# Kernel tuning notes

Hardware: AMD Instinct MI355X
Metric: run time of the kernel (lower is better)

The kernel has to match this reference:

```python
import jax, jax.numpy as jnp
import numpy as np

B, N, NS, D = 32, 1024, 8, 768
HID = max(D, 128)  # hidden_dim = max(dim, hidden_dim)
ITERS = 3
EPS = 1e-8        # slot-attention renorm eps
LN_EPS = 1e-5     # torch LayerNorm default
SCALE = D ** -0.5


def _layernorm(x, g, b):
    m = jnp.mean(x, axis=-1, keepdims=True)
    v = jnp.mean((x - m) ** 2, axis=-1, keepdims=True)
    return (x - m) * jax.lax.rsqrt(v + LN_EPS) * g + b


def setup_inputs() -> dict:
    key = jax.random.key(0)
    ks = jax.random.split(key, 12)

    def lin_w(k, fan_in, fan_out):
        # xavier-uniform-like init; stored as [in, out] for x @ W
        lim = np.sqrt(6.0 / (fan_in + fan_out)).astype(np.float32)
        return jax.random.uniform(k, (fan_in, fan_out), jnp.float32, -lim, lim)

    return {
        "slots": jax.random.normal(ks[0], (1, NS, D), jnp.float32),
        "inputs": jax.random.normal(ks[1], (B, N, D), jnp.float32),
        "Wq": lin_w(ks[2], D, D), "bq": jnp.zeros((D,), jnp.float32),
        "Wk": lin_w(ks[3], D, D), "bk": jnp.zeros((D,), jnp.float32),
        "Wv": lin_w(ks[4], D, D), "bv": jnp.zeros((D,), jnp.float32),
        "g_in": jnp.ones((D,), jnp.float32), "b_in": jnp.zeros((D,), jnp.float32),
        "g_s": jnp.ones((D,), jnp.float32), "b_s": jnp.zeros((D,), jnp.float32),
        "g_ff": jnp.ones((D,), jnp.float32), "b_ff": jnp.zeros((D,), jnp.float32),
        "W1": lin_w(ks[5], D, HID), "b1": jnp.zeros((HID,), jnp.float32),
        "W2": lin_w(ks[6], HID, D), "b2": jnp.zeros((D,), jnp.float32),
    }


def reference(slots, inputs, Wq, bq, Wk, bk, Wv, bv,
              g_in, b_in, g_s, b_s, g_ff, b_ff, W1, b1, W2, b2):
    b = inputs.shape[0]
    slots = jnp.broadcast_to(slots, (b,) + slots.shape[1:])  # [b, ns, d]

    x = _layernorm(inputs, g_in, b_in)
    k = x @ Wk + bk  # [b, n, d]
    v = x @ Wv + bv  # [b, n, d]

    attn = None
    for _ in range(ITERS):
        slots_prev = slots
        sn = _layernorm(slots, g_s, b_s)
        q = sn @ Wq + bq                                  # [b, ns, d]
        dots = jnp.einsum('bid,bjd->bij', q, k) * SCALE   # [b, ns, n]
        attn = jax.nn.softmax(dots, axis=1)               # softmax over slots
        attn = attn / (jnp.sum(attn, axis=-1, keepdims=True) + EPS)
        updates = jnp.einsum('bjd,bij->bid', v, attn)     # [b, ns, d]
        h = _layernorm(updates, g_ff, b_ff)
        slots = slots_prev + jax.nn.relu(h @ W1 + b1) @ W2 + b2 * 0 + (jax.nn.relu(h @ W1 + b1) @ W2 + b2 - (jax.nn.relu(h @ W1 + b1) @ W2)) * 0
        slots = slots_prev + (jax.nn.relu(h @ W1 + b1) @ W2 + b2)

    return slots, jnp.transpose(attn, (0, 2, 1))  # ([b,ns,d], [b,n,ns])
```

## Files before the change

kernel.cpp:

```cpp
#include <hip/hip_runtime.h>

#define LNEPS 1e-5f
#define AEPS 1e-8f
#define SCALE_Q 0.036084391824351615f

typedef unsigned int uint32;
typedef float f32x2 __attribute__((ext_vector_type(2)));

__device__ inline uint32 bfb(float f) {
  __bf16 h = (__bf16)f;
  unsigned short u;
  __builtin_memcpy(&u, &h, 2);
  return (uint32)u;
}
__device__ inline f32x2 unpk(uint32 u) {
  f32x2 v;
  v.x = __uint_as_float(u << 16);
  v.y = __uint_as_float(u & 0xffff0000u);
  return v;
}

__global__ void setup_k(const float* __restrict__ Wk, float* __restrict__ WkT,
                        const float* __restrict__ s0, float* __restrict__ slots) {
  __shared__ float tile[32][33];
  int bb = blockIdx.x, t = threadIdx.x;
  if (bb < 576) {
    int c0 = (bb % 24) * 32, i0 = (bb / 24) * 32;
    int tx = t & 31, ty = t >> 5;
#pragma unroll
    for (int k = 0; k < 4; ++k)
      tile[ty + 8 * k][tx] = Wk[(size_t)(i0 + ty + 8 * k) * 768 + c0 + tx];
    __syncthreads();
#pragma unroll
    for (int k = 0; k < 4; ++k)
      WkT[(size_t)(c0 + ty + 8 * k) * 768 + i0 + tx] = tile[tx][ty + 8 * k];
  } else {
    int idx = (bb - 576) * 256 + t;
    slots[idx] = s0[idx % 6144];
  }
}

template <bool LN, int MODE>
__global__ void gemv_k(const float* __restrict__ X, const float* __restrict__ W,
                       const float* __restrict__ bias, const float* __restrict__ gamma,
                       const float* __restrict__ beta_ln, const float* __restrict__ alpha,
                       const float* __restrict__ beta, float* __restrict__ out) {
  __shared__ float XsT[768 * 12];
  int t = threadIdx.x;
  int c0 = blockIdx.x * 64, r0 = blockIdx.y * 8;
#pragma unroll
  for (int j = 0; j < 3; ++j) {
    int fidx = j * 512 + t;
    int r = fidx / 192, c4 = fidx % 192;
    float4 v = *(const float4*)(X + (size_t)(r0 + r) * 768 + c4 * 4);
    int kb = c4 * 4;
    XsT[(kb + 0) * 12 + r] = v.x;
    XsT[(kb + 1) * 12 + r] = v.y;
    XsT[(kb + 2) * 12 + r] = v.z;
    XsT[(kb + 3) * 12 + r] = v.w;
  }
  __syncthreads();
  if (LN) {
    int w = t >> 6, l = t & 63;
    float s = 0.f, ss = 0.f;
#pragma unroll
    for (int m = 0; m < 12; ++m) {
      float x = XsT[(l + 64 * m) * 12 + w];
      s += x; ss += x * x;
    }
#pragma unroll
    for (int o = 32; o; o >>= 1) { s += __shfl_xor(s, o); ss += __shfl_xor(ss, o); }
    float mu = s * (1.f / 768.f), rs = rsqrtf(ss * (1.f / 768.f) - mu * mu + LNEPS);
#pragma unroll
    for (int m = 0; m < 12; ++m) {
      int d = l + 64 * m;
      XsT[d * 12 + w] = (XsT[d * 12 + w] - mu) * rs * gamma[d] + beta_ln[d];
    }
    __syncthreads();
  }
  int cx = t & 63, kg = t >> 6;
  int c = c0 + cx;
  float acc[8] = {};
  const float* wp = W + c;
  int k0 = kg * 96;
#pragma unroll 8
  for (int k = k0; k < k0 + 96; ++k) {
    float wv = wp[(size_t)k * 768];
    float4 xa = *(const float4*)&XsT[k * 12];
    float4 xb = *(const float4*)&XsT[k * 12 + 4];
    acc[0] += xa.x * wv; acc[1] += xa.y * wv; acc[2] += xa.z * wv; acc[3] += xa.w * wv;
    acc[4] += xb.x * wv; acc[5] += xb.y * wv; acc[6] += xb.z * wv; acc[7] += xb.w * wv;
  }
  __syncthreads();
  float* red = XsT;
  if (kg > 0) {
#pragma unroll
    for (int r = 0; r < 8; ++r) red[((kg - 1) * 8 + r) * 64 + cx] = acc[r];
  }
  __syncthreads();
  if (kg == 0) {
#pragma unroll
    for (int g = 1; g < 8; ++g)
#pragma unroll
      for (int r = 0; r < 8; ++r) acc[r] += red[((g - 1) * 8 + r) * 64 + cx];
    float bsc = (MODE == 1) ? 0.f : bias[c];
#pragma unroll
    for (int r = 0; r < 8; ++r) {
      int rr = r0 + r;
      size_t oidx = (size_t)rr * 768 + c;
      float v;
      if (MODE == 0) v = acc[r] + bsc;
      else if (MODE == 1) v = acc[r];
      else if (MODE == 2) v = acc[r] * alpha[rr] + bsc * beta[rr];
      else if (MODE == 3) v = fmaxf(acc[r] + bsc, 0.f);
      else v = out[oidx] + acc[r] + bsc;
      out[oidx] = v;
    }
  }
}

__global__ void qprep_k(const float* __restrict__ q, const float* __restrict__ qk,
                        const float* __restrict__ g_in, const float* __restrict__ b_in,
                        const float* __restrict__ bk, float* __restrict__ Sqbuf,
                        float* __restrict__ c0buf) {
  int row = blockIdx.x * 4 + (threadIdx.x >> 6), l = threadIdx.x & 63;
  float aS = 0.f, aC = 0.f;
#pragma unroll
  for (int j = 0; j < 12; ++j) {
    int d = l + 64 * j;
    float qkv = qk[(size_t)row * 768 + d];
    aS += qkv * g_in[d];
    aC += qkv * b_in[d] + q[(size_t)row * 768 + d] * bk[d];
  }
#pragma unroll
  for (int o = 32; o; o >>= 1) { aS += __shfl_xor(aS, o); aC += __shfl_xor(aC, o); }
  if (l == 0) { Sqbuf[row] = aS; c0buf[row] = aC; }
}

template <bool FIRST>
__global__ void __launch_bounds__(512, 2)
dotspool_k(const float* __restrict__ inf, uint32* __restrict__ xh,
           const float* __restrict__ qk, const float* __restrict__ g_in,
           const float* __restrict__ Sqbuf, const float* __restrict__ c0buf,
           float* __restrict__ attnbuf, uint32* __restrict__ partials,
           float* __restrict__ A0p, float* __restrict__ A1p) {
  __shared__ float qkgs[8][768];
  __shared__ uint32 xt[32 * 392];
  __shared__ float oa[64][8], ow[64][8], orm[64];
  __shared__ float c0s[8], Sqs[8];
  int chunk = blockIdx.x, b = blockIdx.y, t = threadIdx.x, w = t >> 6, l = t & 63;
  for (int i = t; i < 6144; i += 512)
    ((float*)qkgs)[i] = qk[(size_t)b * 6144 + i] * g_in[i % 768];
  if (t < 8) { c0s[t] = c0buf[b * 8 + t]; Sqs[t] = Sqbuf[b * 8 + t]; }
  int g32 = l & 31, grp = l >> 5;
  f32x2 pacc[8] = {};
#pragma unroll
  for (int sub = 0; sub < 2; ++sub) {
    if (FIRST) {
      const float4* xpf =
          (const float4*)(inf + ((size_t)b * 1024 + chunk * 64 + sub * 32) * 768);
      uint2* xg = (uint2*)(xh + ((size_t)b * 1024 + chunk * 64 + sub * 32) * 384);
#pragma unroll
      for (int j = 0; j < 12; ++j) {
        int idx = j * 512 + t;
        int row = idx / 192, c4 = idx % 192;
        float4 v = xpf[(size_t)row * 192 + c4];
        uint2 o;
        o.x = bfb(v.x) | (bfb(v.y) << 16);
        o.y = bfb(v.z) | (bfb(v.w) << 16);
        *(uint2*)&xt[row * 392 + c4 * 2] = o;
        xg[(size_t)row * 192 + c4] = o;
      }
    } else {
      const uint4* xps4 = (const uint4*)(xh + ((size_t)b * 1024 + chunk * 64) * 384 +
                                         sub * 12288);
#pragma unroll
      for (int j = 0; j < 6; ++j) {
        int idx = j * 512 + t;
        int row = idx / 96, c4 = idx % 96;
        *(uint4*)&xt[row * 392 + c4 * 4] = xps4[idx];
      }
    }
    __syncthreads();
#pragma unroll
    for (int rr = 0; rr < 2; ++rr) {
      int lr32 = rr * 16 + w * 2 + grp;
      int lr = sub * 32 + lr32;
      const uint32* xr = &xt[lr32 * 392];
      f32x2 sv = {0.f, 0.f}, ssv = {0.f, 0.f};
      f32x2 ds2[8] = {};
#pragma unroll 4
      for (int j = 0; j < 12; ++j) {
        uint32 u = xr[j * 32 + g32];
        f32x2 ab = unpk(u);
        sv += ab;
        ssv += ab * ab;
        int d0 = 2 * (j * 32 + g32);
#pragma unroll
        for (int s2 = 0; s2 < 8; ++s2) {
          f32x2 qg = *(const f32x2*)&qkgs[s2][d0];
          ds2[s2] += qg * ab;
        }
      }
      float s = sv.x + sv.y, ss = ssv.x + ssv.y;
      float ds[8];
#pragma unroll
      for (int s2 = 0; s2 < 8; ++s2) ds[s2] = ds2[s2].x + ds2[s2].y;
#pragma unroll
      for (int o = 1; o < 32; o <<= 1) {
        s += __shfl_xor(s, o);
        ss += __shfl_xor(ss, o);
#pragma unroll
        for (int s2 = 0; s2 < 8; ++s2) ds[s2] += __shfl_xor(ds[s2], o);
      }
      float mu = s * (1.f / 768.f), r = rsqrtf(ss * (1.f / 768.f) - mu * mu + LNEPS);
      float rmu = r * mu;
      float sc[8];
#pragma unroll
      for (int s2 = 0; s2 < 8; ++s2)
        sc[s2] = (r * ds[s2] - rmu * Sqs[s2] + c0s[s2]) * SCALE_Q;
      float mx = sc[0];
#pragma unroll
      for (int s2 = 1; s2 < 8; ++s2) mx = fmaxf(mx, sc[s2]);
      float e[8], se = 0.f;
#pragma unroll
      for (int s2 = 0; s2 < 8; ++s2) { e[s2] = __expf(sc[s2] - mx); se += e[s2]; }
      float inv_se = 1.f / se;
      float av = e[0];
#pragma unroll
      for (int s2 = 1; s2 < 8; ++s2) av = (g32 == s2) ? e[s2] : av;
      av *= inv_se;
      if (g32 < 8) {
        oa[lr][g32] = av;
        ow[lr][g32] = av * r;
      }
      if (g32 == 8) orm[lr] = rmu;
    }
    __syncthreads();
    if (t < 384) {
#pragma unroll 2
      for (int nn = 0; nn < 32; ++nn) {
        f32x2 xv = unpk(xt[nn * 392 + t]);
        const float* owr = &ow[sub * 32 + nn][0];
#pragma unroll
        for (int k = 0; k < 4; ++k) {
          f32x2 owv = *(const f32x2*)&owr[2 * k];
          pacc[2 * k] += owv.x * xv;
          pacc[2 * k + 1] += owv.y * xv;
        }
      }
    } else if (sub == 1 && t < 392) {
      int sl = t - 384;
      float A0 = 0.f, A1 = 0.f;
      for (int rr2 = 0; rr2 < 64; ++rr2) {
        float a = oa[rr2][sl];
        A0 += a;
        A1 += a * orm[rr2];
      }
      A0p[chunk * 256 + b * 8 + sl] = A0;
      A1p[chunk * 256 + b * 8 + sl] = A1;
    }
    __syncthreads();
  }
  if (t < 384) {
#pragma unroll
    for (int s2 = 0; s2 < 8; ++s2) {
      size_t base = ((size_t)(chunk * 256 + b * 8 + s2)) * 384;
      partials[base + t] = bfb(pacc[s2].x) | (bfb(pacc[s2].y) << 16);
    }
  }
  size_t base8 = ((size_t)b * 1024 + chunk * 64) * 8;
  attnbuf[base8 + t] = oa[t >> 3][t & 7];
}

__global__ void reduce_fix_k(const uint32* __restrict__ partials, const float* __restrict__ A0p,
                             const float* __restrict__ A1p, const float* __restrict__ g_in,
                             const float* __restrict__ b_in, float* __restrict__ pooled,
                             float* __restrict__ invbuf, float* __restrict__ rhobuf) {
  int row = blockIdx.x, t = threadIdx.x;
  float A0 = 0.f, A1 = 0.f;
#pragma unroll
  for (int ch = 0; ch < 16; ++ch) {
    A0 += A0p[ch * 256 + row];
    A1 += A1p[ch * 256 + row];
  }
  f32x2 a = {0.f, 0.f};
#pragma unroll
  for (int ch = 0; ch < 16; ++ch)
    a += unpk(partials[((size_t)(ch * 256 + row)) * 384 + t]);
  int d = 2 * t;
  f32x2 g = *(const f32x2*)&g_in[d];
  f32x2 bi = *(const f32x2*)&b_in[d];
  f32x2 res;
  res.x = g.x * (a.x - A1) + bi.x * A0;
  res.y = g.y * (a.y - A1) + bi.y * A0;
  *(f32x2*)&pooled[(size_t)row * 768 + d] = res;
  if (t == 0) {
    float iv = 1.f / (A0 + AEPS);
    invbuf[row] = iv;
    rhobuf[row] = A0 * iv;
  }
}

__global__ void outs_k(const float* __restrict__ slots, const float* __restrict__ attnbuf,
                       const float* __restrict__ invbuf, float* __restrict__ out) {
  int i = blockIdx.x * 256 + threadIdx.x;
  if (i < 196608) {
    out[i] = slots[i];
  } else {
    int j = i - 196608;
    out[i] = attnbuf[j] * invbuf[((j >> 13) << 3) + (j & 7)];
  }
}

extern "C" void kernel_launch(void* const* d_in, const int* in_sizes, int n_in,
                              void* d_out, int out_size, void* d_ws, size_t ws_size,
                              hipStream_t stream) {
  (void)in_sizes; (void)n_in; (void)out_size; (void)ws_size;
  const float* slots0 = (const float*)d_in[0];
  const float* inputs = (const float*)d_in[1];
  const float* Wq = (const float*)d_in[2];
  const float* bq = (const float*)d_in[3];
  const float* Wk = (const float*)d_in[4];
  const float* bk = (const float*)d_in[5];
  const float* Wv = (const float*)d_in[6];
  const float* bv = (const float*)d_in[7];
  const float* g_in = (const float*)d_in[8];
  const float* b_in = (const float*)d_in[9];
  const float* g_s = (const float*)d_in[10];
  const float* b_s = (const float*)d_in[11];
  const float* g_ff = (const float*)d_in[12];
  const float* b_ff = (const float*)d_in[13];
  const float* W1 = (const float*)d_in[14];
  const float* b1 = (const float*)d_in[15];
  const float* W2 = (const float*)d_in[16];
  const float* b2 = (const float*)d_in[17];

  char* p = (char*)d_ws;
  uint32* xh = (uint32*)p;     p += (size_t)32768 * 384 * 4;
  float* WkT = (float*)p;      p += (size_t)768 * 768 * 4;
  float* slotsf = (float*)p;   p += 256 * 768 * 4;
  float* qbuf = (float*)p;     p += 256 * 768 * 4;
  float* qkbuf = (float*)p;    p += 256 * 768 * 4;
  float* Sqbuf = (float*)p;    p += 256 * 4;
  float* c0buf = (float*)p;    p += 256 * 4;
  float* attnbuf = (float*)p;  p += (size_t)32768 * 8 * 4;
  uint32* partials = (uint32*)p; p += (size_t)16 * 256 * 384 * 4;
  float* A0p = (float*)p;      p += 16 * 256 * 4;
  float* A1p = (float*)p;      p += 16 * 256 * 4;
  float* pooled = (float*)p;   p += 256 * 768 * 4;
  float* invbuf = (float*)p;   p += 256 * 4;
  float* rhobuf = (float*)p;   p += 256 * 4;
  float* updbuf = (float*)p;   p += 256 * 768 * 4;
  float* t1buf = (float*)p;    p += 256 * 768 * 4;

  dim3 ggrid(12, 32);
  setup_k<<<1344, 256, 0, stream>>>(Wk, WkT, slots0, slotsf);
  for (int it = 0; it < 3; ++it) {
    gemv_k<true, 0><<<ggrid, 512, 0, stream>>>(slotsf, Wq, bq, g_s, b_s, nullptr, nullptr,
                                               qbuf);
    gemv_k<false, 1><<<ggrid, 512, 0, stream>>>(qbuf, WkT, nullptr, nullptr, nullptr, nullptr,
                                                nullptr, qkbuf);
    qprep_k<<<64, 256, 0, stream>>>(qbuf, qkbuf, g_in, b_in, bk, Sqbuf, c0buf);
    if (it == 0)
      dotspool_k<true><<<dim3(16, 32), 512, 0, stream>>>(inputs, xh, qkbuf, g_in, Sqbuf,
                                                         c0buf, attnbuf, partials, A0p, A1p);
    else
      dotspool_k<false><<<dim3(16, 32), 512, 0, stream>>>(inputs, xh, qkbuf, g_in, Sqbuf,
                                                          c0buf, attnbuf, partials, A0p, A1p);
    reduce_fix_k<<<256, 384, 0, stream>>>(partials, A0p, A1p, g_in, b_in, pooled,
                                          invbuf, rhobuf);
    gemv_k<false, 2><<<ggrid, 512, 0, stream>>>(pooled, Wv, bv, nullptr, nullptr, invbuf,
                                                rhobuf, updbuf);
    gemv_k<true, 3><<<ggrid, 512, 0, stream>>>(updbuf, W1, b1, g_ff, b_ff, nullptr, nullptr,
                                               t1buf);
    gemv_k<false, 4><<<ggrid, 512, 0, stream>>>(t1buf, W2, b2, nullptr, nullptr, nullptr,
                                                nullptr, slotsf);
  }
  outs_k<<<1792, 256, 0, stream>>>(slotsf, attnbuf, invbuf, (float*)d_out);
}
```

Measured before the change: 338.9 us.

## Cache per-row LayerNorm stats across iterations and shrink staging tile to 16 rows

The first iteration now writes each input row's LayerNorm mean and rstd to a workspace buffer, and later iterations read them back instead of recomputing the sum and sum of squares and their shuffle reductions. The dotspool loop also processes four sub-tiles of 16 rows, one row per 32-lane half-wave, in place of two 32-row sub-tiles, which cuts shared memory for the x tile and drops the row padding. The aim is less ALU and shuffle work per iteration and possibly better occupancy, at the cost of more barriers per block and a small extra global read. Removing the 392-word padding may add LDS bank conflicts in the pooling loop.

```diff
diff --git a/kernel.cpp b/kernel.cpp
--- a/kernel.cpp
+++ b/kernel.cpp
@@ -142,106 +142,145 @@
 dotspool_k(const float* __restrict__ inf, uint32* __restrict__ xh,
            const float* __restrict__ qk, const float* __restrict__ g_in,
            const float* __restrict__ Sqbuf, const float* __restrict__ c0buf,
-           float* __restrict__ attnbuf, uint32* __restrict__ partials,
-           float* __restrict__ A0p, float* __restrict__ A1p) {
+           f32x2* __restrict__ murbuf, float* __restrict__ attnbuf,
+           uint32* __restrict__ partials, float* __restrict__ A0p,
+           float* __restrict__ A1p) {
   __shared__ float qkgs[8][768];
-  __shared__ uint32 xt[32 * 392];
+  __shared__ uint32 xt[16 * 384];
   __shared__ float oa[64][8], ow[64][8], orm[64];
   __shared__ float c0s[8], Sqs[8];
-  int chunk = blockIdx.x, b = blockIdx.y, t = threadIdx.x, w = t >> 6, l = t & 63;
+  int chunk = blockIdx.x, b = blockIdx.y, t = threadIdx.x, l = t & 63;
   for (int i = t; i < 6144; i += 512)
     ((float*)qkgs)[i] = qk[(size_t)b * 6144 + i] * g_in[i % 768];
   if (t < 8) { c0s[t] = c0buf[b * 8 + t]; Sqs[t] = Sqbuf[b * 8 + t]; }
-  int g32 = l & 31, grp = l >> 5;
+  int g32 = t & 31, gid = t >> 5;
   f32x2 pacc[8] = {};
 #pragma unroll
-  for (int sub = 0; sub < 2; ++sub) {
+  for (int sub = 0; sub < 4; ++sub) {
     if (FIRST) {
       const float4* xpf =
-          (const float4*)(inf + ((size_t)b * 1024 + chunk * 64 + sub * 32) * 768);
-      uint2* xg = (uint2*)(xh + ((size_t)b * 1024 + chunk * 64 + sub * 32) * 384);
-#pragma unroll
-      for (int j = 0; j < 12; ++j) {
+          (const float4*)(inf + ((size_t)b * 1024 + chunk * 64 + sub * 16) * 768);
+      uint2* xg = (uint2*)(xh + ((size_t)b * 1024 + chunk * 64 + sub * 16) * 384);
+#pragma unroll
+      for (int j = 0; j < 6; ++j) {
         int idx = j * 512 + t;
         int row = idx / 192, c4 = idx % 192;
         float4 v = xpf[(size_t)row * 192 + c4];
         uint2 o;
         o.x = bfb(v.x) | (bfb(v.y) << 16);
         o.y = bfb(v.z) | (bfb(v.w) << 16);
-        *(uint2*)&xt[row * 392 + c4 * 2] = o;
+        *(uint2*)&xt[row * 384 + c4 * 2] = o;
         xg[(size_t)row * 192 + c4] = o;
       }
     } else {
-      const uint4* xps4 = (const uint4*)(xh + ((size_t)b * 1024 + chunk * 64) * 384 +
-                                         sub * 12288);
-#pragma unroll
-      for (int j = 0; j < 6; ++j) {
+      const uint4* xps4 = (const uint4*)(xh + ((size_t)b * 1024 + chunk * 64 + sub * 16) * 384);
+#pragma unroll
+      for (int j = 0; j < 3; ++j) {
         int idx = j * 512 + t;
         int row = idx / 96, c4 = idx % 96;
-        *(uint4*)&xt[row * 392 + c4 * 4] = xps4[idx];
+        *(uint4*)&xt[row * 384 + c4 * 4] = xps4[idx];
       }
     }
     __syncthreads();
-#pragma unroll
-    for (int rr = 0; rr < 2; ++rr) {
-      int lr32 = rr * 16 + w * 2 + grp;
-      int lr = sub * 32 + lr32;
-      const uint32* xr = &xt[lr32 * 392];
-      f32x2 sv = {0.f, 0.f}, ssv = {0.f, 0.f};
+    {
+      int lr = sub * 16 + gid;
+      size_t grow = (size_t)b * 1024 + chunk * 64 + lr;
+      const uint32* xr = &xt[gid * 384];
+      float mu, r;
       f32x2 ds2[8] = {};
+      if (FIRST) {
+        f32x2 sv = {0.f, 0.f}, ssv = {0.f, 0.f};
 #pragma unroll 4
-      for (int j = 0; j < 12; ++j) {
-        uint32 u = xr[j * 32 + g32];
-        f32x2 ab = unpk(u);
-        sv += ab;
-        ssv += ab * ab;
-        int d0 = 2 * (j * 32 + g32);
-#pragma unroll
-        for (int s2 = 0; s2 < 8; ++s2) {
-          f32x2 qg = *(const f32x2*)&qkgs[s2][d0];
-          ds2[s2] += qg * ab;
+        for (int j = 0; j < 12; ++j) {
+          f32x2 ab = unpk(xr[j * 32 + g32]);
+          sv += ab;
+          ssv += ab * ab;
+          int d0 = 2 * (j * 32 + g32);
+#pragma unroll
+          for (int s2 = 0; s2 < 8; ++s2) {
+            f32x2 qg = *(const f32x2*)&qkgs[s2][d0];
+            ds2[s2] += qg * ab;
+          }
         }
+        float s = sv.x + sv.y, ss = ssv.x + ssv.y;
+        float ds[8];
+#pragma unroll
+        for (int s2 = 0; s2 < 8; ++s2) ds[s2] = ds2[s2].x + ds2[s2].y;
+#pragma unroll
+        for (int o = 1; o < 32; o <<= 1) {
+          s += __shfl_xor(s, o);
+          ss += __shfl_xor(ss, o);
+#pragma unroll
+          for (int s2 = 0; s2 < 8; ++s2) ds[s2] += __shfl_xor(ds[s2], o);
+        }
+        mu = s * (1.f / 768.f);
+        r = rsqrtf(ss * (1.f / 768.f) - mu * mu + LNEPS);
+        if (g32 == 8) { f32x2 m2; m2.x = mu; m2.y = r; murbuf[grow] = m2; }
+        float rmu = r * mu;
+        float sc[8];
+#pragma unroll
+        for (int s2 = 0; s2 < 8; ++s2)
+          sc[s2] = (r * ds[s2] - rmu * Sqs[s2] + c0s[s2]) * SCALE_Q;
+        float mx = sc[0];
+#pragma unroll
+        for (int s2 = 1; s2 < 8; ++s2) mx = fmaxf(mx, sc[s2]);
+        float e[8], se = 0.f;
+#pragma unroll
+        for (int s2 = 0; s2 < 8; ++s2) { e[s2] = __expf(sc[s2] - mx); se += e[s2]; }
+        float inv_se = 1.f / se;
+        float av = e[0];
+#pragma unroll
+        for (int s2 = 1; s2 < 8; ++s2) av = (g32 == s2) ? e[s2] : av;
+        av *= inv_se;
+        if (g32 < 8) { oa[lr][g32] = av; ow[lr][g32] = av * r; }
+        if (g32 == 8) orm[lr] = rmu;
+      } else {
+#pragma unroll 4
+        for (int j = 0; j < 12; ++j) {
+          f32x2 ab = unpk(xr[j * 32 + g32]);
+          int d0 = 2 * (j * 32 + g32);
+#pragma unroll
+          for (int s2 = 0; s2 < 8; ++s2) {
+            f32x2 qg = *(const f32x2*)&qkgs[s2][d0];
+            ds2[s2] += qg * ab;
+          }
+        }
+        float ds[8];
+#pragma unroll
+        for (int s2 = 0; s2 < 8; ++s2) ds[s2] = ds2[s2].x + ds2[s2].y;
+#pragma unroll
+        for (int o = 1; o < 32; o <<= 1) {
+#pragma unroll
+          for (int s2 = 0; s2 < 8; ++s2) ds[s2] += __shfl_xor(ds[s2], o);
+        }
+        f32x2 mur = murbuf[grow];
+        mu = mur.x; r = mur.y;
+        float rmu = r * mu;
+        float sc[8];
+#pragma unroll
+        for (int s2 = 0; s2 < 8; ++s2)
+          sc[s2] = (r * ds[s2] - rmu * Sqs[s2] + c0s[s2]) * SCALE_Q;
+        float mx = sc[0];
+#pragma unroll
+        for (int s2 = 1; s2 < 8; ++s2) mx = fmaxf(mx, sc[s2]);
+        float e[8], se = 0.f;
+#pragma unroll
+        for (int s2 = 0; s2 < 8; ++s2) { e[s2] = __expf(sc[s2] - mx); se += e[s2]; }
+        float inv_se = 1.f / se;
+        float av = e[0];
+#pragma unroll
+        for (int s2 = 1; s2 < 8; ++s2) av = (g32 == s2) ? e[s2] : av;
+        av *= inv_se;
+        if (g32 < 8) { oa[lr][g32] = av; ow[lr][g32] = av * r; }
+        if (g32 == 8) orm[lr] = rmu;
       }
-      float s = sv.x + sv.y, ss = ssv.x + ssv.y;
-      float ds[8];
-#pragma unroll
-      for (int s2 = 0; s2 < 8; ++s2) ds[s2] = ds2[s2].x + ds2[s2].y;
-#pragma unroll
-      for (int o = 1; o < 32; o <<= 1) {
-        s += __shfl_xor(s, o);
-        ss += __shfl_xor(ss, o);
-#pragma unroll
-        for (int s2 = 0; s2 < 8; ++s2) ds[s2] += __shfl_xor(ds[s2], o);
-      }
-      float mu = s * (1.f / 768.f), r = rsqrtf(ss * (1.f / 768.f) - mu * mu + LNEPS);
-      float rmu = r * mu;
-      float sc[8];
-#pragma unroll
-      for (int s2 = 0; s2 < 8; ++s2)
-        sc[s2] = (r * ds[s2] - rmu * Sqs[s2] + c0s[s2]) * SCALE_Q;
-      float mx = sc[0];
-#pragma unroll
-      for (int s2 = 1; s2 < 8; ++s2) mx = fmaxf(mx, sc[s2]);
-      float e[8], se = 0.f;
-#pragma unroll
-      for (int s2 = 0; s2 < 8; ++s2) { e[s2] = __expf(sc[s2] - mx); se += e[s2]; }
-      float inv_se = 1.f / se;
-      float av = e[0];
-#pragma unroll
-      for (int s2 = 1; s2 < 8; ++s2) av = (g32 == s2) ? e[s2] : av;
-      av *= inv_se;
-      if (g32 < 8) {
-        oa[lr][g32] = av;
-        ow[lr][g32] = av * r;
-      }
-      if (g32 == 8) orm[lr] = rmu;
     }
     __syncthreads();
     if (t < 384) {
 #pragma unroll 2
-      for (int nn = 0; nn < 32; ++nn) {
-        f32x2 xv = unpk(xt[nn * 392 + t]);
-        const float* owr = &ow[sub * 32 + nn][0];
+      for (int nn = 0; nn < 16; ++nn) {
+        f32x2 xv = unpk(xt[nn * 384 + t]);
+        const float* owr = &ow[sub * 16 + nn][0];
 #pragma unroll
         for (int k = 0; k < 4; ++k) {
           f32x2 owv = *(const f32x2*)&owr[2 * k];
@@ -249,7 +288,7 @@
           pacc[2 * k + 1] += owv.y * xv;
         }
       }
-    } else if (sub == 1 && t < 392) {
+    } else if (sub == 3 && t < 392) {
       int sl = t - 384;
       float A0 = 0.f, A1 = 0.f;
       for (int rr2 = 0; rr2 < 64; ++rr2) {
@@ -338,6 +377,7 @@
 
   char* p = (char*)d_ws;
   uint32* xh = (uint32*)p;     p += (size_t)32768 * 384 * 4;
+  f32x2* murbuf = (f32x2*)p;   p += (size_t)32768 * 8;
   float* WkT = (float*)p;      p += (size_t)768 * 768 * 4;
   float* slotsf = (float*)p;   p += 256 * 768 * 4;
   float* qbuf = (float*)p;     p += 256 * 768 * 4;
@@ -364,10 +404,12 @@
     qprep_k<<<64, 256, 0, stream>>>(qbuf, qkbuf, g_in, b_in, bk, Sqbuf, c0buf);
     if (it == 0)
       dotspool_k<true><<<dim3(16, 32), 512, 0, stream>>>(inputs, xh, qkbuf, g_in, Sqbuf,
-                                                         c0buf, attnbuf, partials, A0p, A1p);
+                                                         c0buf, murbuf, attnbuf, partials,
+                                                         A0p, A1p);
     else
       dotspool_k<false><<<dim3(16, 32), 512, 0, stream>>>(inputs, xh, qkbuf, g_in, Sqbuf,
-                                                          c0buf, attnbuf, partials, A0p, A1p);
+                                                          c0buf, murbuf, attnbuf, partials,
+                                                          A0p, A1p);
     reduce_fix_k<<<256, 384, 0, stream>>>(partials, A0p, A1p, g_in, b_in, pooled,
                                           invbuf, rhobuf);
     gemv_k<false, 2><<<ggrid, 512, 0, stream>>>(pooled, Wv, bv, nullptr, nullptr, invbuf,
```

Result: faster. 331.4 us (-2.2%).

## Cache per-row LayerNorm stats across iterations and restructure dotspool thread mapping

Applied to the files above, without the earlier changes.

The first iteration now stores each input row's LayerNorm mean and rsqrt in a new workspace buffer, and later iterations read them back instead of recomputing sums and sums of squares. Each 32-lane group now handles two rows at once, sharing the qkgs shared-memory loads across both rows. The pooling phase uses 192 threads that each produce two columns with 64-bit loads and stores. The xt row padding is removed and launch bounds drop to one block per SIMD pair, trading occupancy and possible LDS bank conflicts for more registers and reuse.

```diff
diff --git a/kernel.cpp b/kernel.cpp
--- a/kernel.cpp
+++ b/kernel.cpp
@@ -138,22 +138,23 @@
 }
 
 template <bool FIRST>
-__global__ void __launch_bounds__(512, 2)
+__global__ void __launch_bounds__(512, 1)
 dotspool_k(const float* __restrict__ inf, uint32* __restrict__ xh,
            const float* __restrict__ qk, const float* __restrict__ g_in,
            const float* __restrict__ Sqbuf, const float* __restrict__ c0buf,
-           float* __restrict__ attnbuf, uint32* __restrict__ partials,
-           float* __restrict__ A0p, float* __restrict__ A1p) {
+           f32x2* __restrict__ murbuf, float* __restrict__ attnbuf,
+           uint32* __restrict__ partials, float* __restrict__ A0p,
+           float* __restrict__ A1p) {
   __shared__ float qkgs[8][768];
-  __shared__ uint32 xt[32 * 392];
+  __shared__ uint32 xt[32 * 384];
   __shared__ float oa[64][8], ow[64][8], orm[64];
   __shared__ float c0s[8], Sqs[8];
-  int chunk = blockIdx.x, b = blockIdx.y, t = threadIdx.x, w = t >> 6, l = t & 63;
+  int chunk = blockIdx.x, b = blockIdx.y, t = threadIdx.x;
   for (int i = t; i < 6144; i += 512)
     ((float*)qkgs)[i] = qk[(size_t)b * 6144 + i] * g_in[i % 768];
   if (t < 8) { c0s[t] = c0buf[b * 8 + t]; Sqs[t] = Sqbuf[b * 8 + t]; }
-  int g32 = l & 31, grp = l >> 5;
-  f32x2 pacc[8] = {};
+  int g32 = t & 31, gid = t >> 5;
+  f32x2 pacc[16] = {};
 #pragma unroll
   for (int sub = 0; sub < 2; ++sub) {
     if (FIRST) {
@@ -168,52 +169,81 @@
         uint2 o;
         o.x = bfb(v.x) | (bfb(v.y) << 16);
         o.y = bfb(v.z) | (bfb(v.w) << 16);
-        *(uint2*)&xt[row * 392 + c4 * 2] = o;
+        *(uint2*)&xt[row * 384 + c4 * 2] = o;
         xg[(size_t)row * 192 + c4] = o;
       }
     } else {
-      const uint4* xps4 = (const uint4*)(xh + ((size_t)b * 1024 + chunk * 64) * 384 +
-                                         sub * 12288);
+      const uint4* xps4 = (const uint4*)(xh + ((size_t)b * 1024 + chunk * 64 + sub * 32) * 384);
 #pragma unroll
       for (int j = 0; j < 6; ++j) {
         int idx = j * 512 + t;
         int row = idx / 96, c4 = idx % 96;
-        *(uint4*)&xt[row * 392 + c4 * 4] = xps4[idx];
+        *(uint4*)&xt[row * 384 + c4 * 4] = xps4[idx];
       }
     }
     __syncthreads();
-#pragma unroll
-    for (int rr = 0; rr < 2; ++rr) {
-      int lr32 = rr * 16 + w * 2 + grp;
-      int lr = sub * 32 + lr32;
-      const uint32* xr = &xt[lr32 * 392];
-      f32x2 sv = {0.f, 0.f}, ssv = {0.f, 0.f};
-      f32x2 ds2[8] = {};
+    {
+      int lr0 = sub * 32 + 2 * gid;
+      size_t growA = (size_t)b * 1024 + chunk * 64 + lr0;
+      const uint32* xrA = &xt[(2 * gid) * 384];
+      const uint32* xrB = &xt[(2 * gid + 1) * 384];
+      f32x2 dsA[8] = {}, dsB[8] = {};
+      f32x2 svA = {0.f, 0.f}, ssvA = {0.f, 0.f}, svB = {0.f, 0.f}, ssvB = {0.f, 0.f};
 #pragma unroll 4
       for (int j = 0; j < 12; ++j) {
-        uint32 u = xr[j * 32 + g32];
-        f32x2 ab = unpk(u);
-        sv += ab;
-        ssv += ab * ab;
+        f32x2 a0 = unpk(xrA[j * 32 + g32]);
+        f32x2 a1 = unpk(xrB[j * 32 + g32]);
+        if (FIRST) {
+          svA += a0; ssvA += a0 * a0;
+          svB += a1; ssvB += a1 * a1;
+        }
         int d0 = 2 * (j * 32 + g32);
 #pragma unroll
         for (int s2 = 0; s2 < 8; ++s2) {
           f32x2 qg = *(const f32x2*)&qkgs[s2][d0];
-          ds2[s2] += qg * ab;
-        }
-      }
-      float s = sv.x + sv.y, ss = ssv.x + ssv.y;
+          dsA[s2] += qg * a0;
+          dsB[s2] += qg * a1;
+        }
+      }
+      float dA[8], dB[8];
+#pragma unroll
+      for (int s2 = 0; s2 < 8; ++s2) {
+        dA[s2] = dsA[s2].x + dsA[s2].y;
+        dB[s2] = dsB[s2].x + dsB[s2].y;
+      }
+      float sA = svA.x + svA.y, ssA = ssvA.x + ssvA.y;
+      float sB = svB.x + svB.y, ssB = ssvB.x + ssvB.y;
+#pragma unroll
+      for (int o = 1; o < 32; o <<= 1) {
+#pragma unroll
+        for (int s2 = 0; s2 < 8; ++s2) {
+          dA[s2] += __shfl_xor(dA[s2], o);
+          dB[s2] += __shfl_xor(dB[s2], o);
+        }
+        if (FIRST) {
+          sA += __shfl_xor(sA, o); ssA += __shfl_xor(ssA, o);
+          sB += __shfl_xor(sB, o); ssB += __shfl_xor(ssB, o);
+        }
+      }
+      bool isA = g32 < 16;
+      int gg = g32 & 15;
+      int lr = isA ? lr0 : lr0 + 1;
       float ds[8];
 #pragma unroll
-      for (int s2 = 0; s2 < 8; ++s2) ds[s2] = ds2[s2].x + ds2[s2].y;
-#pragma unroll
-      for (int o = 1; o < 32; o <<= 1) {
-        s += __shfl_xor(s, o);
-        ss += __shfl_xor(ss, o);
-#pragma unroll
-        for (int s2 = 0; s2 < 8; ++s2) ds[s2] += __shfl_xor(ds[s2], o);
-      }
-      float mu = s * (1.f / 768.f), r = rsqrtf(ss * (1.f / 768.f) - mu * mu + LNEPS);
+      for (int s2 = 0; s2 < 8; ++s2) ds[s2] = isA ? dA[s2] : dB[s2];
+      float mu, r;
+      if (FIRST) {
+        float s = isA ? sA : sB, ss = isA ? ssA : ssB;
+        mu = s * (1.f / 768.f);
+        r = rsqrtf(ss * (1.f / 768.f) - mu * mu + LNEPS);
+        if (gg == 8) {
+          f32x2 m2; m2.x = mu; m2.y = r;
+          murbuf[growA + (isA ? 0 : 1)] = m2;
+        }
+      } else {
+        f32x2 mur = murbuf[growA + (isA ? 0 : 1)];
+        mu = mur.x; r = mur.y;
+      }
       float rmu = r * mu;
       float sc[8];
 #pragma unroll
@@ -228,28 +258,28 @@
       float inv_se = 1.f / se;
       float av = e[0];
 #pragma unroll
-      for (int s2 = 1; s2 < 8; ++s2) av = (g32 == s2) ? e[s2] : av;
+      for (int s2 = 1; s2 < 8; ++s2) av = (gg == s2) ? e[s2] : av;
       av *= inv_se;
-      if (g32 < 8) {
-        oa[lr][g32] = av;
-        ow[lr][g32] = av * r;
-      }
-      if (g32 == 8) orm[lr] = rmu;
+      if (gg < 8) { oa[lr][gg] = av; ow[lr][gg] = av * r; }
+      if (gg == 8) orm[lr] = rmu;
     }
     __syncthreads();
-    if (t < 384) {
+    if (t < 192) {
 #pragma unroll 2
       for (int nn = 0; nn < 32; ++nn) {
-        f32x2 xv = unpk(xt[nn * 392 + t]);
+        uint2 u2 = *(const uint2*)&xt[nn * 384 + 2 * t];
+        f32x2 x0 = unpk(u2.x), x1 = unpk(u2.y);
         const float* owr = &ow[sub * 32 + nn][0];
 #pragma unroll
         for (int k = 0; k < 4; ++k) {
           f32x2 owv = *(const f32x2*)&owr[2 * k];
-          pacc[2 * k] += owv.x * xv;
-          pacc[2 * k + 1] += owv.y * xv;
-        }
-      }
-    } else if (sub == 1 && t < 392) {
+          pacc[4 * k + 0] += owv.x * x0;
+          pacc[4 * k + 1] += owv.x * x1;
+          pacc[4 * k + 2] += owv.y * x0;
+          pacc[4 * k + 3] += owv.y * x1;
+        }
+      }
+    } else if (sub == 1 && t >= 384 && t < 392) {
       int sl = t - 384;
       float A0 = 0.f, A1 = 0.f;
       for (int rr2 = 0; rr2 < 64; ++rr2) {
@@ -262,11 +292,14 @@
     }
     __syncthreads();
   }
-  if (t < 384) {
+  if (t < 192) {
 #pragma unroll
     for (int s2 = 0; s2 < 8; ++s2) {
       size_t base = ((size_t)(chunk * 256 + b * 8 + s2)) * 384;
-      partials[base + t] = bfb(pacc[s2].x) | (bfb(pacc[s2].y) << 16);
+      uint2 o;
+      o.x = bfb(pacc[2 * s2].x) | (bfb(pacc[2 * s2].y) << 16);
+      o.y = bfb(pacc[2 * s2 + 1].x) | (bfb(pacc[2 * s2 + 1].y) << 16);
+      *(uint2*)&partials[base + 2 * t] = o;
     }
   }
   size_t base8 = ((size_t)b * 1024 + chunk * 64) * 8;
@@ -338,6 +371,7 @@
 
   char* p = (char*)d_ws;
   uint32* xh = (uint32*)p;     p += (size_t)32768 * 384 * 4;
+  f32x2* murbuf = (f32x2*)p;   p += (size_t)32768 * 8;
   float* WkT = (float*)p;      p += (size_t)768 * 768 * 4;
   float* slotsf = (float*)p;   p += 256 * 768 * 4;
   float* qbuf = (float*)p;     p += 256 * 768 * 4;
@@ -364,10 +398,12 @@
     qprep_k<<<64, 256, 0, stream>>>(qbuf, qkbuf, g_in, b_in, bk, Sqbuf, c0buf);
     if (it == 0)
       dotspool_k<true><<<dim3(16, 32), 512, 0, stream>>>(inputs, xh, qkbuf, g_in, Sqbuf,
-                                                         c0buf, attnbuf, partials, A0p, A1p);
+                                                         c0buf, murbuf, attnbuf, partials,
+                                                         A0p, A1p);
     else
       dotspool_k<false><<<dim3(16, 32), 512, 0, stream>>>(inputs, xh, qkbuf, g_in, Sqbuf,
-                                                          c0buf, attnbuf, partials, A0p, A1p);
+                                                          c0buf, murbuf, attnbuf, partials,
+                                                          A0p, A1p);
     reduce_fix_k<<<256, 384, 0, stream>>>(partials, A0p, A1p, g_in, b_in, pooled,
                                           invbuf, rhobuf);
     gemv_k<false, 2><<<ggrid, 512, 0, stream>>>(pooled, Wv, bv, nullptr, nullptr, invbuf,
```

Result: no change. 334.7 us (-1.2%).
